# Kernel tuning notes

Hardware: AMD Instinct MI355X
Metric: run time of the kernel (lower is better)

The kernel has to match this reference:

```python
import jax, jax.numpy as jnp
import numpy as np

Lx, Ly, D, B = 6, 6, 3, 16
SIGMA = 0.5  # keeps the 36-tensor contraction magnitude in fp32 range


def _slice_config(T, s):
    # T: [Lx, Ly, D,D,D,D, 2,2,2,2,2]; bond axes (u,d,l,r), phys axes (self, up, down, left, right)
    sg = s.reshape(Lx, Ly)
    sp = jnp.pad(sg, 1)  # out-of-grid neighbors -> index 0
    ix, iy = jnp.meshgrid(jnp.arange(Lx), jnp.arange(Ly), indexing='ij')
    p = sg
    pu = sp[ix, iy + 1]      # neighbor (x-1, y)
    pd = sp[ix + 2, iy + 1]  # neighbor (x+1, y)
    pl = sp[ix + 1, iy]      # neighbor (x, y-1)
    pr = sp[ix + 1, iy + 2]  # neighbor (x, y+1)
    # advanced indexing: result [Lx, Ly, D, D, D, D] with bond axes (u, d, l, r)
    return T[ix, iy, :, :, :, :, p, pu, pd, pl, pr]


def _amplitude(T, s):
    # exact boundary contraction from ymin (no truncation), equals full .contract()
    A = _slice_config(T, s)            # [Lx, Ly, u, d, l, r]
    Bnd = A[:, 0, :, :, 0, :]          # cap dangling left bonds: [Lx, u, d, r]
    for y in range(1, Ly):
        C = A[:, y]                    # [Lx, u, d, l, r]
        Bnd = jnp.einsum('xabl,xudlr->xaubdr', Bnd, C)
        Bnd = Bnd.reshape(Lx, Bnd.shape[1] * Bnd.shape[2],
                          Bnd.shape[3] * Bnd.shape[4], D)
    M = Bnd[:, :, :, 0]                # cap dangling right bonds: [Lx, chi, chi]
    v = M[0, 0]                        # cap top boundary bond (index 0 of product bond)
    for xx in range(1, Lx):
        v = v @ M[xx]                  # vector-matrix chain down the boundary MPS
    return v[0]                        # cap bottom boundary bond


def setup_inputs() -> dict:
    key = jax.random.key(0)
    kT, kx = jax.random.split(key)
    T = jax.random.normal(kT, (Lx, Ly, D, D, D, D, 2, 2, 2, 2, 2), dtype=jnp.float32) * SIGMA
    x = jax.random.randint(kx, (B, Lx * Ly), 0, 2, dtype=jnp.int32)
    return {"x": x, "T": T}


def reference(x, T):
    # batched amplitudes: [B]
    return jax.vmap(lambda s: _amplitude(T, s))(x)
```

## Files before the change

kernel.cpp:

```cpp
#include <hip/hip_runtime.h>


constexpr int SITE_STRIDE = 81 * 32;

__global__ __launch_bounds__(256)
void peps_amp_kernel(const int* __restrict__ xs, const float* __restrict__ T,
                     float* __restrict__ out) {
    __shared__ float A[36 * 81];
    __shared__ float V[729];
    __shared__ float Wbuf[2][2187];
    __shared__ int sg[36];
    __shared__ int sidx[36];

    const int b = blockIdx.x;
    const int t = threadIdx.x;

    if (t < 36) sg[t] = xs[b * 36 + t];
    __syncthreads();
    if (t < 36) {
        const int i = t / 6, j = t % 6;
        const int p  = sg[t];
        const int pu = (i > 0) ? sg[t - 6] : 0;
        const int pd = (i < 5) ? sg[t + 6] : 0;
        const int pl = (j > 0) ? sg[t - 1] : 0;
        const int pr = (j < 5) ? sg[t + 1] : 0;
        sidx[t] = (((p * 2 + pu) * 2 + pd) * 2 + pl) * 2 + pr;
    }
    __syncthreads();
    for (int idx = t; idx < 36 * 81; idx += 256) {
        const int site = idx / 81;
        const int perm = idx - site * 81;
        A[idx] = T[site * SITE_STRIDE + perm * 32 + sidx[site]];
    }
    for (int idx = t; idx < 729; idx += 256) V[idx] = (idx == 0) ? 1.0f : 0.0f;
    __syncthreads();

    for (int xc = 0; xc < 6; ++xc) {
        const float* Arow = &A[xc * 6 * 81];

        if (t < 243) {
            const float v0 = V[t], v1 = V[243 + t], v2 = V[486 + t];
            const float* A0 = Arow;
            #pragma unroll
            for (int d = 0; d < 3; ++d)
                #pragma unroll
                for (int r = 0; r < 3; ++r) {
                    Wbuf[0][(d * 3 + r) * 243 + t] =
                        v0 * A0[d * 9 + r] +
                        v1 * A0[27 + d * 9 + r] +
                        v2 * A0[54 + d * 9 + r];
                }
        }
        __syncthreads();

        int cur = 0;
        int P = 81;
        #pragma unroll
        for (int y = 1; y <= 4; ++y) {
            const float* Ay = Arow + y * 81;
            const float* Wp = Wbuf[cur];
            float* Wn = Wbuf[cur ^ 1];
            if (t < 243) {
                const int dc = t / P;
                const int ur = t - dc * P;
                float wv[3][3];
                #pragma unroll
                for (int l = 0; l < 3; ++l)
                    #pragma unroll
                    for (int u = 0; u < 3; ++u)
                        wv[u][l] = Wp[(dc * 3 + l) * 3 * P + u * P + ur];
                #pragma unroll
                for (int d = 0; d < 3; ++d)
                    #pragma unroll
                    for (int r = 0; r < 3; ++r) {
                        float acc = 0.f;
                        #pragma unroll
                        for (int u = 0; u < 3; ++u)
                            #pragma unroll
                            for (int l = 0; l < 3; ++l)
                                acc += wv[u][l] * Ay[((u * 3 + d) * 3 + l) * 3 + r];
                        Wn[((dc * 3 + d) * 3 + r) * P + ur] = acc;
                    }
            }
            __syncthreads();
            cur ^= 1;
            P /= 3;
        }

        {
            const float* Ay = Arow + 5 * 81;
            const float* Wp = Wbuf[cur];
            if (t < 243) {
                float wv[3][3];
                #pragma unroll
                for (int l = 0; l < 3; ++l)
                    #pragma unroll
                    for (int u = 0; u < 3; ++u)
                        wv[u][l] = Wp[(t * 3 + l) * 3 + u];
                #pragma unroll
                for (int d = 0; d < 3; ++d) {
                    float acc = 0.f;
                    #pragma unroll
                    for (int u = 0; u < 3; ++u)
                        #pragma unroll
                        for (int l = 0; l < 3; ++l)
                            acc += wv[u][l] * Ay[u * 27 + d * 9 + l * 3];
                    V[t * 3 + d] = acc;
                }
            }
        }
        __syncthreads();
    }

    if (t == 0) out[b] = V[0];
}

extern "C" void kernel_launch(void* const* d_in, const int* in_sizes, int n_in,
                              void* d_out, int out_size, void* d_ws, size_t ws_size,
                              hipStream_t stream) {
    const int* xs = (const int*)d_in[0];
    const float* T = (const float*)d_in[1];
    float* out = (float*)d_out;
    const int B = in_sizes[0] / 36;
    peps_amp_kernel<<<B, 256, 0, stream>>>(xs, T, out);
}
```

Measured before the change: 76.95 us.

## Contract PEPS from top and bottom simultaneously and meet in the middle

Splits the row-by-row boundary contraction into two halves run by separate 256-thread groups in one 512-thread block. One half sweeps downward from row 0 and the other sweeps upward from row 5, with bond roles swapped. The first boundary row is built directly by a per-thread chain product instead of starting from a unit vector. The two boundary vectors are then combined with an inner product and a wave reduction. This roughly halves the serial chain of synchronised contraction steps, at the cost of twice the shared memory and a final reduction.

```diff
diff --git a/kernel.cpp b/kernel.cpp
--- a/kernel.cpp
+++ b/kernel.cpp
@@ -3,17 +3,20 @@
 
 constexpr int SITE_STRIDE = 81 * 32;
 
-__global__ __launch_bounds__(256)
+__global__ __launch_bounds__(512)
 void peps_amp_kernel(const int* __restrict__ xs, const float* __restrict__ T,
                      float* __restrict__ out) {
     __shared__ float A[36 * 81];
-    __shared__ float V[729];
-    __shared__ float Wbuf[2][2187];
+    __shared__ float Vsh[2][729];
+    __shared__ float Wsh[2][2][2187];
+    __shared__ float red[8];
     __shared__ int sg[36];
     __shared__ int sidx[36];
 
     const int b = blockIdx.x;
     const int t = threadIdx.x;
+    const int half = t >> 8;
+    const int lt = t & 255;
 
     if (t < 36) sg[t] = xs[b * 36 + t];
     __syncthreads();
@@ -27,28 +30,61 @@
         sidx[t] = (((p * 2 + pu) * 2 + pd) * 2 + pl) * 2 + pr;
     }
     __syncthreads();
-    for (int idx = t; idx < 36 * 81; idx += 256) {
+    for (int idx = t; idx < 36 * 81; idx += 512) {
         const int site = idx / 81;
         const int perm = idx - site * 81;
         A[idx] = T[site * SITE_STRIDE + perm * 32 + sidx[site]];
     }
-    for (int idx = t; idx < 729; idx += 256) V[idx] = (idx == 0) ? 1.0f : 0.0f;
     __syncthreads();
 
-    for (int xc = 0; xc < 6; ++xc) {
+    float* V  = Vsh[half];
+    float* Wa = Wsh[half][0];
+    float* Wb = Wsh[half][1];
+    const int SS = half ? 9 : 27;
+    const int SO = half ? 27 : 9;
+
+    {
+        const float* Arow = &A[(half ? 30 : 0) * 81];
+        for (int k = lt; k < 729; k += 256) {
+            int c[6];
+            c[0] = k / 243;
+            c[1] = (k / 81) % 3;
+            c[2] = (k / 27) % 3;
+            c[3] = (k / 9) % 3;
+            c[4] = (k / 3) % 3;
+            c[5] = k % 3;
+            float v0 = Arow[c[0] * SO + 0];
+            float v1 = Arow[c[0] * SO + 1];
+            float v2 = Arow[c[0] * SO + 2];
+            #pragma unroll
+            for (int y = 1; y <= 4; ++y) {
+                const float* Ay = Arow + y * 81 + c[y] * SO;
+                const float n0 = v0 * Ay[0] + v1 * Ay[3] + v2 * Ay[6];
+                const float n1 = v0 * Ay[1] + v1 * Ay[4] + v2 * Ay[7];
+                const float n2 = v0 * Ay[2] + v1 * Ay[5] + v2 * Ay[8];
+                v0 = n0; v1 = n1; v2 = n2;
+            }
+            const float* A5 = Arow + 5 * 81 + c[5] * SO;
+            V[k] = v0 * A5[0] + v1 * A5[3] + v2 * A5[6];
+        }
+    }
+    __syncthreads();
+
+    for (int cc = 0; cc < 2; ++cc) {
+        const int xc = half ? (4 - cc) : (1 + cc);
         const float* Arow = &A[xc * 6 * 81];
 
-        if (t < 243) {
-            const float v0 = V[t], v1 = V[243 + t], v2 = V[486 + t];
+        if (lt < 243) {
+            const float v0 = V[lt], v1 = V[243 + lt], v2 = V[486 + lt];
             const float* A0 = Arow;
             #pragma unroll
-            for (int d = 0; d < 3; ++d)
+            for (int o = 0; o < 3; ++o)
                 #pragma unroll
                 for (int r = 0; r < 3; ++r) {
-                    Wbuf[0][(d * 3 + r) * 243 + t] =
-                        v0 * A0[d * 9 + r] +
-                        v1 * A0[27 + d * 9 + r] +
-                        v2 * A0[54 + d * 9 + r];
+                    Wa[(o * 3 + r) * 243 + lt] =
+                        v0 * A0[o * SO + r] +
+                        v1 * A0[SS + o * SO + r] +
+                        v2 * A0[2 * SS + o * SO + r];
                 }
         }
         __syncthreads();
@@ -58,28 +94,28 @@
         #pragma unroll
         for (int y = 1; y <= 4; ++y) {
             const float* Ay = Arow + y * 81;
-            const float* Wp = Wbuf[cur];
-            float* Wn = Wbuf[cur ^ 1];
-            if (t < 243) {
-                const int dc = t / P;
-                const int ur = t - dc * P;
+            const float* Wp = cur ? Wb : Wa;
+            float* Wn = cur ? Wa : Wb;
+            if (lt < 243) {
+                const int dc = lt / P;
+                const int ur = lt - dc * P;
                 float wv[3][3];
                 #pragma unroll
                 for (int l = 0; l < 3; ++l)
                     #pragma unroll
-                    for (int u = 0; u < 3; ++u)
-                        wv[u][l] = Wp[(dc * 3 + l) * 3 * P + u * P + ur];
+                    for (int s = 0; s < 3; ++s)
+                        wv[s][l] = Wp[(dc * 3 + l) * 3 * P + s * P + ur];
                 #pragma unroll
-                for (int d = 0; d < 3; ++d)
+                for (int o = 0; o < 3; ++o)
                     #pragma unroll
                     for (int r = 0; r < 3; ++r) {
                         float acc = 0.f;
                         #pragma unroll
-                        for (int u = 0; u < 3; ++u)
+                        for (int s = 0; s < 3; ++s)
                             #pragma unroll
                             for (int l = 0; l < 3; ++l)
-                                acc += wv[u][l] * Ay[((u * 3 + d) * 3 + l) * 3 + r];
-                        Wn[((dc * 3 + d) * 3 + r) * P + ur] = acc;
+                                acc += wv[s][l] * Ay[s * SS + o * SO + l * 3 + r];
+                        Wn[((dc * 3 + o) * 3 + r) * P + ur] = acc;
                     }
             }
             __syncthreads();
@@ -89,30 +125,41 @@
 
         {
             const float* Ay = Arow + 5 * 81;
-            const float* Wp = Wbuf[cur];
-            if (t < 243) {
+            const float* Wp = cur ? Wb : Wa;
+            if (lt < 243) {
                 float wv[3][3];
                 #pragma unroll
                 for (int l = 0; l < 3; ++l)
                     #pragma unroll
-                    for (int u = 0; u < 3; ++u)
-                        wv[u][l] = Wp[(t * 3 + l) * 3 + u];
+                    for (int s = 0; s < 3; ++s)
+                        wv[s][l] = Wp[(lt * 3 + l) * 3 + s];
                 #pragma unroll
-                for (int d = 0; d < 3; ++d) {
+                for (int o = 0; o < 3; ++o) {
                     float acc = 0.f;
                     #pragma unroll
-                    for (int u = 0; u < 3; ++u)
+                    for (int s = 0; s < 3; ++s)
                         #pragma unroll
                         for (int l = 0; l < 3; ++l)
-                            acc += wv[u][l] * Ay[u * 27 + d * 9 + l * 3];
-                    V[t * 3 + d] = acc;
+                            acc += wv[s][l] * Ay[s * SS + o * SO + l * 3];
+                    V[lt * 3 + o] = acc;
                 }
             }
         }
         __syncthreads();
     }
 
-    if (t == 0) out[b] = V[0];
+    float partial = 0.f;
+    for (int i = t; i < 729; i += 512) partial += Vsh[0][i] * Vsh[1][i];
+    #pragma unroll
+    for (int off = 32; off > 0; off >>= 1) partial += __shfl_down(partial, off);
+    if ((t & 63) == 0) red[t >> 6] = partial;
+    __syncthreads();
+    if (t == 0) {
+        float s = 0.f;
+        #pragma unroll
+        for (int w = 0; w < 8; ++w) s += red[w];
+        out[b] = s;
+    }
 }
 
 extern "C" void kernel_launch(void* const* d_in, const int* in_sizes, int n_in,
@@ -122,5 +169,5 @@
     const float* T = (const float*)d_in[1];
     float* out = (float*)d_out;
     const int B = in_sizes[0] / 36;
-    peps_amp_kernel<<<B, 256, 0, stream>>>(xs, T, out);
+    peps_amp_kernel<<<B, 512, 0, stream>>>(xs, T, out);
 }
```

Result: faster. 68.49 us (-11.0%).
